# Performance work log

Measured on AMD Instinct MI355X. Metric: run time of the kernel, lower is better.

The kernel has to match this reference:

```python
import jax, jax.numpy as jnp
import numpy as np

N_HEADS = 16
NEG_INF = -1e30


def setup_inputs() -> dict:
    key = jax.random.key(0)
    ks = jax.random.split(key, 5)
    B, S, D = 2, 2048, 2048
    scale_w = 1.0 / np.sqrt(D)  # keep activations well-scaled
    return {
        "x": jax.random.normal(ks[0], (B, S, D), dtype=jnp.float32),
        "Wq": jax.random.normal(ks[1], (D, D), dtype=jnp.float32) * scale_w,
        "Wk": jax.random.normal(ks[2], (D, D), dtype=jnp.float32) * scale_w,
        "Wv": jax.random.normal(ks[3], (D, D), dtype=jnp.float32) * scale_w,
        "Wo": jax.random.normal(ks[4], (D, D), dtype=jnp.float32) * scale_w,
    }


def reference(x, Wq, Wk, Wv, Wo):
    # Blocked flash attention with online softmax is exactly causal softmax
    # attention; express it directly.
    B, S, D = x.shape
    H = N_HEADS
    dk = D // H
    scale = 1.0 / np.sqrt(dk)

    def heads(w):
        return (x @ w).reshape(B, S, H, dk)

    q = heads(Wq)  # [B,S,H,dk]
    k = heads(Wk)
    v = heads(Wv)

    scores = jnp.einsum("bqhd,bkhd->bhqk", q, k) * scale  # [B,H,S,S]
    causal = jnp.tril(jnp.ones((S, S), dtype=bool))
    scores = jnp.where(causal, scores, NEG_INF)
    p = jax.nn.softmax(scores, axis=-1)
    o = jnp.einsum("bhqk,bkhd->bqhd", p, v).reshape(B, S, D)
    return o @ Wo
```

## Files before the change

kernel.cpp:

```cpp
#include <hip/hip_runtime.h>
#include <hip/hip_bf16.h>

typedef short s16x8 __attribute__((ext_vector_type(8)));
typedef float f32x4 __attribute__((ext_vector_type(4)));
typedef unsigned short u16x4 __attribute__((ext_vector_type(4)));

#define MFMA16(a, b, c) __builtin_amdgcn_mfma_f32_16x16x32_bf16((a), (b), (c), 0, 0, 0)

__device__ __forceinline__ unsigned short f32_to_bf16(float f) {
  unsigned int u = __builtin_bit_cast(unsigned int, f);
  u += 0x7FFFu + ((u >> 16) & 1u);
  return (unsigned short)(u >> 16);
}

__device__ __forceinline__ void glds16(const unsigned short* g, unsigned short* l) {
  __builtin_amdgcn_global_load_lds(
      (const __attribute__((address_space(1))) void*)g,
      (__attribute__((address_space(3))) void*)l, 16, 0, 0);
}

__global__ void cvt_bf16_k(const float* __restrict__ in, unsigned short* __restrict__ out, int n4) {
  int i = blockIdx.x * 256 + threadIdx.x;
  if (i >= n4) return;
  float4 f = ((const float4*)in)[i];
  u16x4 o;
  o.x = f32_to_bf16(f.x); o.y = f32_to_bf16(f.y);
  o.z = f32_to_bf16(f.z); o.w = f32_to_bf16(f.w);
  ((u16x4*)out)[i] = o;
}

__global__ void cvt_t4_k(const float* __restrict__ Wq, const float* __restrict__ Wk,
                         const float* __restrict__ Wv, const float* __restrict__ Wo,
                         unsigned short* __restrict__ outQKV, unsigned short* __restrict__ outO,
                         int D) {
  int z = blockIdx.z;
  const float* in = (z == 0) ? Wq : (z == 1) ? Wk : (z == 2) ? Wv : Wo;
  unsigned short* out = (z < 3) ? (outQKV + (size_t)z * D * D) : outO;
  __shared__ float tile[32][33];
  int tx = threadIdx.x;
  int nt = D >> 5;
  int bx = blockIdx.x % nt;
  int by = blockIdx.x / nt;
  int r = tx >> 3, c4 = (tx & 7) * 4;
  int k0 = by * 32, n0 = bx * 32;
  float4 f = *(const float4*)(in + (size_t)(k0 + r) * D + n0 + c4);
  tile[r][c4 + 0] = f.x; tile[r][c4 + 1] = f.y;
  tile[r][c4 + 2] = f.z; tile[r][c4 + 3] = f.w;
  __syncthreads();
  u16x4 o;
  o.x = f32_to_bf16(tile[c4 + 0][r]);
  o.y = f32_to_bf16(tile[c4 + 1][r]);
  o.z = f32_to_bf16(tile[c4 + 2][r]);
  o.w = f32_to_bf16(tile[c4 + 3][r]);
  *(u16x4*)(out + (size_t)(n0 + r) * D + k0 + c4) = o;
}

template <int OUTF32>
__global__ __launch_bounds__(512, 4) void gemm3b(
    const unsigned short* __restrict__ A, const unsigned short* __restrict__ Bt,
    void* __restrict__ Cv, int M, int N, int K, int ldc) {
  __shared__ unsigned short As[3][256 * 32];
  __shared__ unsigned short Bs[3][128 * 32];
  int t = threadIdx.x, lane = t & 63, w = t >> 6;
  int r16 = lane & 15, kg = lane >> 4;
  int wm = w >> 1, wn = w & 1;
  int nbn = N >> 7;
  int bm = blockIdx.x / nbn, bn = blockIdx.x % nbn;
  const unsigned short* Ag = A + (size_t)bm * 256 * K;
  const unsigned short* Bg = Bt + (size_t)bn * 128 * K;

  const unsigned short* asrc[2];
  int aoff[2];
#pragma unroll
  for (int i = 0; i < 2; ++i) {
    int c = i * 512 + t;
    int row = c >> 2, sl = c & 3;
    asrc[i] = Ag + (size_t)row * K + ((sl ^ ((row >> 1) & 3)) * 8);
    aoff[i] = (i * 512 + (t & ~63)) * 8;
  }
  int brow = t >> 2;
  const unsigned short* bsrc = Bg + (size_t)brow * K + (((t & 3) ^ ((brow >> 1) & 3)) * 8);
  int boff = (t & ~63) * 8;

  auto STAGE = [&](int bi, int kt2) {
    int k0 = kt2 * 32;
    glds16(asrc[0] + k0, &As[bi][aoff[0]]);
    glds16(asrc[1] + k0, &As[bi][aoff[1]]);
    glds16(bsrc + k0, &Bs[bi][boff]);
  };

  f32x4 acc[4][4] = {};
  int nt = K >> 5;
  STAGE(0, 0);
  if (nt > 1) STAGE(1, 1);
  int cur = 0;
  for (int kt = 0; kt < nt; ++kt) {
    if (kt + 1 < nt) {
      asm volatile("s_waitcnt vmcnt(3)" ::: "memory");
    } else {
      asm volatile("s_waitcnt vmcnt(0)" ::: "memory");
    }
    __builtin_amdgcn_s_barrier();
    asm volatile("" ::: "memory");
    if (kt + 2 < nt) {
      int s2 = cur + 2; if (s2 >= 3) s2 -= 3;
      STAGE(s2, kt + 2);
    }
    const unsigned short* Al = As[cur];
    const unsigned short* Bl = Bs[cur];
    s16x8 af[4], bfr[4];
#pragma unroll
    for (int mf = 0; mf < 4; ++mf) {
      int row = wm * 64 + mf * 16 + r16;
      af[mf] = *(const s16x8*)&Al[row * 32 + ((kg ^ ((row >> 1) & 3)) * 8)];
    }
#pragma unroll
    for (int nf = 0; nf < 4; ++nf) {
      int row = wn * 64 + nf * 16 + r16;
      bfr[nf] = *(const s16x8*)&Bl[row * 32 + ((kg ^ ((row >> 1) & 3)) * 8)];
    }
    __builtin_amdgcn_s_setprio(1);
#pragma unroll
    for (int mf = 0; mf < 4; ++mf)
#pragma unroll
      for (int nf = 0; nf < 4; ++nf)
        acc[mf][nf] = MFMA16(af[mf], bfr[nf], acc[mf][nf]);
    __builtin_amdgcn_s_setprio(0);
    cur = (cur == 2) ? 0 : cur + 1;
  }
#pragma unroll
  for (int mf = 0; mf < 4; ++mf)
#pragma unroll
    for (int nf = 0; nf < 4; ++nf)
#pragma unroll
      for (int r = 0; r < 4; ++r) {
        int row = bm * 256 + wm * 64 + mf * 16 + kg * 4 + r;
        int col = bn * 128 + wn * 64 + nf * 16 + r16;
        if (OUTF32)
          ((float*)Cv)[(size_t)row * ldc + col] = acc[mf][nf][r];
        else
          ((unsigned short*)Cv)[(size_t)row * ldc + col] = f32_to_bf16(acc[mf][nf][r]);
      }
}

template <int OUTF32>
__global__ __launch_bounds__(512, 2) void gemm3(
    const unsigned short* __restrict__ A, const unsigned short* __restrict__ Bt,
    void* __restrict__ Cv, int M, int N, int K, int ldc) {
  __shared__ unsigned short As[3][256 * 64];
  __shared__ unsigned short Bs[3][128 * 64];
  int t = threadIdx.x, lane = t & 63, w = t >> 6;
  int r16 = lane & 15, kg = lane >> 4;
  int wm = w >> 1, wn = w & 1;
  int nbn = N >> 7;
  int bm = blockIdx.x / nbn, bn = blockIdx.x % nbn;
  const unsigned short* Ag = A + (size_t)bm * 256 * K;
  const unsigned short* Bg = Bt + (size_t)bn * 128 * K;

  const unsigned short* asrc[4];
  const unsigned short* bsrc[2];
  int aoff[4], boff[2];
#pragma unroll
  for (int i = 0; i < 4; ++i) {
    int c = i * 512 + t;
    int row = c >> 3, sl = c & 7;
    asrc[i] = Ag + (size_t)row * K + ((sl ^ (row & 7)) * 8);
    aoff[i] = (i * 512 + (t & ~63)) * 8;
  }
#pragma unroll
  for (int i = 0; i < 2; ++i) {
    int c = i * 512 + t;
    int row = c >> 3, sl = c & 7;
    bsrc[i] = Bg + (size_t)row * K + ((sl ^ (row & 7)) * 8);
    boff[i] = (i * 512 + (t & ~63)) * 8;
  }

  auto STAGE = [&](int bi, int kt2) {
    int k0 = kt2 * 64;
#pragma unroll
    for (int i = 0; i < 4; ++i) glds16(asrc[i] + k0, &As[bi][aoff[i]]);
#pragma unroll
    for (int i = 0; i < 2; ++i) glds16(bsrc[i] + k0, &Bs[bi][boff[i]]);
  };

  f32x4 acc[4][4] = {};
  int nt = K >> 6;
  STAGE(0, 0);
  if (nt > 1) STAGE(1, 1);
  int cur = 0;
  for (int kt = 0; kt < nt; ++kt) {
    if (kt + 1 < nt) {
      asm volatile("s_waitcnt vmcnt(6)" ::: "memory");
    } else {
      asm volatile("s_waitcnt vmcnt(0)" ::: "memory");
    }
    __builtin_amdgcn_s_barrier();
    asm volatile("" ::: "memory");
    if (kt + 2 < nt) {
      int s2 = cur + 2; if (s2 >= 3) s2 -= 3;
      STAGE(s2, kt + 2);
    }
    const unsigned short* Al = As[cur];
    s16x8 af[4][2], bfr[4][2];
#pragma unroll
    for (int mf = 0; mf < 4; ++mf) {
      int row = wm * 64 + mf * 16 + r16;
#pragma unroll
      for (int ks = 0; ks < 2; ++ks)
        af[mf][ks] = *(const s16x8*)&Al[row * 64 + (((ks * 4 + kg) ^ (row & 7)) * 8)];
    }
#pragma unroll
    for (int nf = 0; nf < 4; ++nf) {
      int row = wn * 64 + nf * 16 + r16;
#pragma unroll
      for (int ks = 0; ks < 2; ++ks)
        bfr[nf][ks] = *(const s16x8*)&Bs[cur][row * 64 + (((ks * 4 + kg) ^ (row & 7)) * 8)];
    }
    __builtin_amdgcn_s_setprio(1);
#pragma unroll
    for (int ks = 0; ks < 2; ++ks)
#pragma unroll
      for (int mf = 0; mf < 4; ++mf)
#pragma unroll
        for (int nf = 0; nf < 4; ++nf)
          acc[mf][nf] = MFMA16(af[mf][ks], bfr[nf][ks], acc[mf][nf]);
    __builtin_amdgcn_s_setprio(0);
    cur = (cur == 2) ? 0 : cur + 1;
  }
#pragma unroll
  for (int mf = 0; mf < 4; ++mf)
#pragma unroll
    for (int nf = 0; nf < 4; ++nf)
#pragma unroll
      for (int r = 0; r < 4; ++r) {
        int row = bm * 256 + wm * 64 + mf * 16 + kg * 4 + r;
        int col = bn * 128 + wn * 64 + nf * 16 + r16;
        if (OUTF32)
          ((float*)Cv)[(size_t)row * ldc + col] = acc[mf][nf][r];
        else
          ((unsigned short*)Cv)[(size_t)row * ldc + col] = f32_to_bf16(acc[mf][nf][r]);
      }
}

__global__ __launch_bounds__(256) void vtr_k(const unsigned short* __restrict__ V,
                                             unsigned short* __restrict__ Vt,
                                             int S, int ld) {
  __shared__ unsigned short T[32 * 128];
  int s0 = blockIdx.x * 32, h = blockIdx.y, b = blockIdx.z;
  int H = gridDim.y;
  int t = threadIdx.x;
  const unsigned short* src = V + (size_t)(b * S + s0) * ld + h * 128;
#pragma unroll
  for (int c = 0; c < 2; ++c) {
    int chunk = c * 256 + t;
    int row = chunk >> 4, slot = chunk & 15;
    glds16(src + (size_t)row * ld + slot * 8, &T[(c * 256 + (t & ~63)) * 8]);
  }
  __syncthreads();
  unsigned short* dst = Vt + ((size_t)(b * H + h) * (S >> 3) + (s0 >> 3)) * 1024;
#pragma unroll
  for (int c = 0; c < 2; ++c) {
    int oc = c * 256 + t;
    int sl = oc >> 7, d = oc & 127;
    s16x8 v;
#pragma unroll
    for (int j = 0; j < 8; ++j) v[j] = (short)T[(sl * 8 + j) * 128 + d];
    *(s16x8*)(dst + (size_t)oc * 8) = v;
  }
}

__global__ __launch_bounds__(512) void attn2_k(
    const unsigned short* __restrict__ Q, const unsigned short* __restrict__ Kx,
    const unsigned short* __restrict__ Vt, unsigned short* __restrict__ O,
    int S, int D, int Bn, int ld) {
  const float scale = 0.08838834764831843f;
  int hb = blockIdx.x;
  int h = hb / Bn, b = hb % Bn;
  int NQ = S >> 7;
  int qt = NQ - 1 - blockIdx.y;
  int H = D >> 7;
  int t = threadIdx.x, lane = t & 63, w = t >> 6;
  int r16 = lane & 15, kg = lane >> 4;
  const unsigned short* Qb  = Q + (size_t)b * S * ld + h * 128;
  const unsigned short* Kb  = Kx + (size_t)b * S * ld + h * 128;
  const unsigned short* Vtb = Vt + (size_t)(b * H + h) * (S >> 3) * 1024;

  __shared__ unsigned short Kbuf[2][64 * 128];
  __shared__ unsigned short Vbuf[2][64 * 128];
  __shared__ unsigned short Pl[8][16 * 64];

  auto STAGE = [&](int bufi, int kv0) {
    const unsigned short* Ksrc = Kb + (size_t)kv0 * ld;
#pragma unroll
    for (int c = 0; c < 2; ++c) {
      int chunk = c * 512 + t;
      int row = chunk >> 4, slot = chunk & 15;
      glds16(Ksrc + (size_t)row * ld + ((slot ^ (row & 7)) * 8),
             &Kbuf[bufi][(c * 512 + (t & ~63)) * 8]);
    }
    const unsigned short* Vsrc = Vtb + (size_t)(kv0 >> 3) * 1024;
#pragma unroll
    for (int c = 0; c < 2; ++c) {
      int chunk = c * 512 + t;
      glds16(Vsrc + (size_t)chunk * 8, &Vbuf[bufi][(c * 512 + (t & ~63)) * 8]);
    }
  };

  int W0 = qt * 128 + w * 16;
  int qg = W0 + r16;
  s16x8 qf[4];
#pragma unroll
  for (int ks = 0; ks < 4; ++ks)
    qf[ks] = *(const s16x8*)(Qb + (size_t)qg * ld + ks * 32 + kg * 8);
  f32x4 oacc[8] = {};
  float m_st = -1e30f, l_st = 0.f;
  int nt = (qt + 1) * 2;
  int cur = 0;
  STAGE(0, 0);
  __syncthreads();
  for (int it = 0; it < nt; ++it) {
    int kv0 = it * 64;
    if (it + 1 < nt) STAGE(cur ^ 1, (it + 1) * 64);
    const unsigned short* Kl = Kbuf[cur];
    const unsigned short* Vl = Vbuf[cur];
    if (kv0 <= W0 + 15) {
      f32x4 st4[4];
      __builtin_amdgcn_s_setprio(1);
#pragma unroll
      for (int kf = 0; kf < 4; ++kf) {
        f32x4 s = {};
#pragma unroll
        for (int ks = 0; ks < 4; ++ks) {
          int row = kf * 16 + r16;
          s16x8 kfr = *(const s16x8*)&Kl[row * 128 + (((ks * 4 + kg) ^ (row & 7)) * 8)];
          s = MFMA16(kfr, qf[ks], s);
        }
        st4[kf] = s;
      }
      __builtin_amdgcn_s_setprio(0);
      float p[4][4];
      float mx = -1e30f;
#pragma unroll
      for (int kf = 0; kf < 4; ++kf)
#pragma unroll
        for (int r = 0; r < 4; ++r) {
          int kvg = kv0 + kf * 16 + kg * 4 + r;
          float sv = st4[kf][r] * scale;
          sv = (kvg <= qg) ? sv : -1e30f;
          p[kf][r] = sv;
          mx = fmaxf(mx, sv);
        }
      mx = fmaxf(mx, __shfl_xor(mx, 16, 64));
      mx = fmaxf(mx, __shfl_xor(mx, 32, 64));
      bool skip = __all(mx <= m_st);
      float m_new = skip ? m_st : fmaxf(m_st, mx);
      float rs = 0.f;
#pragma unroll
      for (int kf = 0; kf < 4; ++kf)
#pragma unroll
        for (int r = 0; r < 4; ++r) {
          float e = __expf(p[kf][r] - m_new);
          p[kf][r] = e;
          rs += e;
        }
      rs += __shfl_xor(rs, 16, 64);
      rs += __shfl_xor(rs, 32, 64);
#pragma unroll
      for (int kf = 0; kf < 4; ++kf) {
        unsigned int lo = (unsigned int)f32_to_bf16(p[kf][0]) | ((unsigned int)f32_to_bf16(p[kf][1]) << 16);
        unsigned int hi = (unsigned int)f32_to_bf16(p[kf][2]) | ((unsigned int)f32_to_bf16(p[kf][3]) << 16);
        int sslot = 2 * kf + (kg >> 1);
        int base = r16 * 64 + ((sslot ^ (r16 & 7)) * 8) + (kg & 1) * 4;
        *(unsigned int*)&Pl[w][base]     = lo;
        *(unsigned int*)&Pl[w][base + 2] = hi;
      }
      asm volatile("s_waitcnt lgkmcnt(0)" ::: "memory");
      __builtin_amdgcn_sched_barrier(0);
      if (!skip) {
        float alpha = __expf(m_st - m_new);
        l_st = l_st * alpha + rs;
        m_st = m_new;
        float ar[4];
#pragma unroll
        for (int r = 0; r < 4; ++r) ar[r] = __shfl(alpha, kg * 4 + r, 64);
#pragma unroll
        for (int f = 0; f < 8; ++f)
#pragma unroll
          for (int r = 0; r < 4; ++r) oacc[f][r] *= ar[r];
      } else {
        l_st += rs;
      }
      __builtin_amdgcn_s_setprio(1);
#pragma unroll
      for (int tt = 0; tt < 2; ++tt) {
        s16x8 pf = *(const s16x8*)&Pl[w][r16 * 64 + (((4 * tt + kg) ^ (r16 & 7)) * 8)];
#pragma unroll
        for (int f = 0; f < 8; ++f) {
          s16x8 vf = *(const s16x8*)&Vl[((4 * tt + kg) * 128 + f * 16 + r16) * 8];
          oacc[f] = MFMA16(pf, vf, oacc[f]);
        }
      }
      __builtin_amdgcn_s_setprio(0);
    }
    __syncthreads();
    cur ^= 1;
  }
  float linv = 1.0f / l_st;
  float lr[4];
#pragma unroll
  for (int r = 0; r < 4; ++r) lr[r] = __shfl(linv, kg * 4 + r, 64);
#pragma unroll
  for (int f = 0; f < 8; ++f)
#pragma unroll
    for (int r = 0; r < 4; ++r) {
      size_t idx = ((size_t)b * S + W0 + kg * 4 + r) * D + h * 128 + f * 16 + r16;
      O[idx] = f32_to_bf16(oacc[f][r] * lr[r]);
    }
}

extern "C" void kernel_launch(void* const* d_in, const int* in_sizes, int n_in,
                              void* d_out, int out_size, void* d_ws, size_t ws_size,
                              hipStream_t stream) {
  const float* x  = (const float*)d_in[0];
  const float* Wq = (const float*)d_in[1];
  const float* Wk = (const float*)d_in[2];
  const float* Wv = (const float*)d_in[3];
  const float* Wo = (const float*)d_in[4];
  const int D = 2048, H = 16;
  const int M = in_sizes[0] / D;
  const int B = 2, S = M / B;
  const int LD = 3 * D;

  unsigned short* xb    = (unsigned short*)d_ws;
  unsigned short* Wqkvt = xb + (size_t)M * D;
  unsigned short* Wot   = Wqkvt + (size_t)3 * D * D;
  unsigned short* QKVb  = Wot + (size_t)D * D;
  unsigned short* Ob    = xb;
  unsigned short* VtA   = Wqkvt;

  int n4 = M * D / 4;
  cvt_bf16_k<<<(n4 + 255) / 256, 256, 0, stream>>>(x, xb, n4);
  int tgrid = (D / 32) * (D / 32);
  cvt_t4_k<<<dim3(tgrid, 1, 4), 256, 0, stream>>>(Wq, Wk, Wv, Wo, Wqkvt, Wot, D);

  gemm3b<0><<<(M / 256) * (LD / 128), 512, 0, stream>>>(xb, Wqkvt, QKVb, M, LD, D, LD);

  vtr_k<<<dim3(S / 32, H, B), 256, 0, stream>>>(QKVb + 2 * D, VtA, S, LD);

  attn2_k<<<dim3(H * B, S / 128), 512, 0, stream>>>(QKVb, QKVb + D, VtA, Ob, S, D, B, LD);

  gemm3<1><<<(M / 256) * (D / 128), 512, 0, stream>>>(Ob, Wot, d_out, M, D, D, D);
}
```

Baseline: 277.5 us.

## Retile output projection GEMM to 128x128 tiles with 256 threads and K=32 stages

Replaces the output-projection GEMM (256x128 tiles, 512 threads, K-step 64) with a 128x128 tile, 256-thread variant that stages 32-wide K slices in a triple buffer with a new XOR swizzle. For M=4096, N=2048 this doubles the block count from 128 to 256, which should fill more of the GPU's compute units, and the smaller LDS footprint allows three blocks per CU. The trade-off is less data reuse per tile, and twice as many barrier-synchronised K iterations with only one MFMA k-step each, which raises sync and load-issue overhead.

```diff
diff --git a/kernel.cpp b/kernel.cpp
--- a/kernel.cpp
+++ b/kernel.cpp
@@ -144,53 +144,48 @@
 }
 
 template <int OUTF32>
-__global__ __launch_bounds__(512, 2) void gemm3(
+__global__ __launch_bounds__(256, 3) void gemm3c(
     const unsigned short* __restrict__ A, const unsigned short* __restrict__ Bt,
     void* __restrict__ Cv, int M, int N, int K, int ldc) {
-  __shared__ unsigned short As[3][256 * 64];
-  __shared__ unsigned short Bs[3][128 * 64];
+  __shared__ unsigned short As[3][128 * 32];
+  __shared__ unsigned short Bs[3][128 * 32];
   int t = threadIdx.x, lane = t & 63, w = t >> 6;
   int r16 = lane & 15, kg = lane >> 4;
   int wm = w >> 1, wn = w & 1;
   int nbn = N >> 7;
   int bm = blockIdx.x / nbn, bn = blockIdx.x % nbn;
-  const unsigned short* Ag = A + (size_t)bm * 256 * K;
+  const unsigned short* Ag = A + (size_t)bm * 128 * K;
   const unsigned short* Bg = Bt + (size_t)bn * 128 * K;
 
-  const unsigned short* asrc[4];
+  const unsigned short* asrc[2];
   const unsigned short* bsrc[2];
-  int aoff[4], boff[2];
-#pragma unroll
-  for (int i = 0; i < 4; ++i) {
-    int c = i * 512 + t;
-    int row = c >> 3, sl = c & 7;
-    asrc[i] = Ag + (size_t)row * K + ((sl ^ (row & 7)) * 8);
-    aoff[i] = (i * 512 + (t & ~63)) * 8;
-  }
+  int doff[2];
 #pragma unroll
   for (int i = 0; i < 2; ++i) {
-    int c = i * 512 + t;
-    int row = c >> 3, sl = c & 7;
-    bsrc[i] = Bg + (size_t)row * K + ((sl ^ (row & 7)) * 8);
-    boff[i] = (i * 512 + (t & ~63)) * 8;
+    int c = i * 256 + t;
+    int row = c >> 2, sl = c & 3;
+    int col = (sl ^ ((row >> 1) & 3)) * 8;
+    asrc[i] = Ag + (size_t)row * K + col;
+    bsrc[i] = Bg + (size_t)row * K + col;
+    doff[i] = (i * 256 + (t & ~63)) * 8;
   }
 
   auto STAGE = [&](int bi, int kt2) {
-    int k0 = kt2 * 64;
-#pragma unroll
-    for (int i = 0; i < 4; ++i) glds16(asrc[i] + k0, &As[bi][aoff[i]]);
-#pragma unroll
-    for (int i = 0; i < 2; ++i) glds16(bsrc[i] + k0, &Bs[bi][boff[i]]);
+    int k0 = kt2 * 32;
+    glds16(asrc[0] + k0, &As[bi][doff[0]]);
+    glds16(asrc[1] + k0, &As[bi][doff[1]]);
+    glds16(bsrc[0] + k0, &Bs[bi][doff[0]]);
+    glds16(bsrc[1] + k0, &Bs[bi][doff[1]]);
   };
 
   f32x4 acc[4][4] = {};
-  int nt = K >> 6;
+  int nt = K >> 5;
   STAGE(0, 0);
   if (nt > 1) STAGE(1, 1);
   int cur = 0;
   for (int kt = 0; kt < nt; ++kt) {
     if (kt + 1 < nt) {
-      asm volatile("s_waitcnt vmcnt(6)" ::: "memory");
+      asm volatile("s_waitcnt vmcnt(4)" ::: "memory");
     } else {
       asm volatile("s_waitcnt vmcnt(0)" ::: "memory");
     }
@@ -201,29 +196,24 @@
       STAGE(s2, kt + 2);
     }
     const unsigned short* Al = As[cur];
-    s16x8 af[4][2], bfr[4][2];
+    const unsigned short* Bl = Bs[cur];
+    s16x8 af[4], bfr[4];
 #pragma unroll
     for (int mf = 0; mf < 4; ++mf) {
       int row = wm * 64 + mf * 16 + r16;
-#pragma unroll
-      for (int ks = 0; ks < 2; ++ks)
-        af[mf][ks] = *(const s16x8*)&Al[row * 64 + (((ks * 4 + kg) ^ (row & 7)) * 8)];
+      af[mf] = *(const s16x8*)&Al[row * 32 + ((kg ^ ((row >> 1) & 3)) * 8)];
     }
 #pragma unroll
     for (int nf = 0; nf < 4; ++nf) {
       int row = wn * 64 + nf * 16 + r16;
-#pragma unroll
-      for (int ks = 0; ks < 2; ++ks)
-        bfr[nf][ks] = *(const s16x8*)&Bs[cur][row * 64 + (((ks * 4 + kg) ^ (row & 7)) * 8)];
+      bfr[nf] = *(const s16x8*)&Bl[row * 32 + ((kg ^ ((row >> 1) & 3)) * 8)];
     }
     __builtin_amdgcn_s_setprio(1);
 #pragma unroll
-    for (int ks = 0; ks < 2; ++ks)
-#pragma unroll
-      for (int mf = 0; mf < 4; ++mf)
-#pragma unroll
-        for (int nf = 0; nf < 4; ++nf)
-          acc[mf][nf] = MFMA16(af[mf][ks], bfr[nf][ks], acc[mf][nf]);
+    for (int mf = 0; mf < 4; ++mf)
+#pragma unroll
+      for (int nf = 0; nf < 4; ++nf)
+        acc[mf][nf] = MFMA16(af[mf], bfr[nf], acc[mf][nf]);
     __builtin_amdgcn_s_setprio(0);
     cur = (cur == 2) ? 0 : cur + 1;
   }
@@ -233,7 +223,7 @@
     for (int nf = 0; nf < 4; ++nf)
 #pragma unroll
       for (int r = 0; r < 4; ++r) {
-        int row = bm * 256 + wm * 64 + mf * 16 + kg * 4 + r;
+        int row = bm * 128 + wm * 64 + mf * 16 + kg * 4 + r;
         int col = bn * 128 + wn * 64 + nf * 16 + r16;
         if (OUTF32)
           ((float*)Cv)[(size_t)row * ldc + col] = acc[mf][nf][r];
@@ -449,5 +439,5 @@
 
   attn2_k<<<dim3(H * B, S / 128), 512, 0, stream>>>(QKVb, QKVb + D, VtA, Ob, S, D, B, LD);
 
-  gemm3<1><<<(M / 256) * (D / 128), 512, 0, stream>>>(Ob, Wot, d_out, M, D, D, D);
-}
+  gemm3c<1><<<(M / 128) * (D / 128), 256, 0, stream>>>(Ob, Wot, d_out, M, D, D, D);
+}
```

Measured after the change: 281.1 us. No clear change (+1.3%).

## Give each attention wave two 16-row query tiles to reuse K/V fragments

Applied to the files above, without the earlier changes.

The attention kernel now runs 4 waves of 256 threads instead of 8 waves of 512. Each wave handles 32 query rows as two 16-row tiles, so every K and V fragment read from LDS feeds two MFMAs instead of one. This halves LDS fragment traffic per MFMA. In exchange it doubles per-wave accumulator registers, gives fewer waves to hide latency, and staging work per thread goes up.

```diff
diff --git a/kernel.cpp b/kernel.cpp
--- a/kernel.cpp
+++ b/kernel.cpp
@@ -269,7 +269,7 @@
   }
 }
 
-__global__ __launch_bounds__(512) void attn2_k(
+__global__ __launch_bounds__(256) void attn4_k(
     const unsigned short* __restrict__ Q, const unsigned short* __restrict__ Kx,
     const unsigned short* __restrict__ Vt, unsigned short* __restrict__ O,
     int S, int D, int Bn, int ld) {
@@ -287,33 +287,34 @@
 
   __shared__ unsigned short Kbuf[2][64 * 128];
   __shared__ unsigned short Vbuf[2][64 * 128];
-  __shared__ unsigned short Pl[8][16 * 64];
+  __shared__ unsigned short Pl[4][32 * 64];
 
   auto STAGE = [&](int bufi, int kv0) {
     const unsigned short* Ksrc = Kb + (size_t)kv0 * ld;
 #pragma unroll
-    for (int c = 0; c < 2; ++c) {
-      int chunk = c * 512 + t;
+    for (int c = 0; c < 4; ++c) {
+      int chunk = c * 256 + t;
       int row = chunk >> 4, slot = chunk & 15;
       glds16(Ksrc + (size_t)row * ld + ((slot ^ (row & 7)) * 8),
-             &Kbuf[bufi][(c * 512 + (t & ~63)) * 8]);
+             &Kbuf[bufi][(c * 256 + (t & ~63)) * 8]);
     }
     const unsigned short* Vsrc = Vtb + (size_t)(kv0 >> 3) * 1024;
 #pragma unroll
-    for (int c = 0; c < 2; ++c) {
-      int chunk = c * 512 + t;
-      glds16(Vsrc + (size_t)chunk * 8, &Vbuf[bufi][(c * 512 + (t & ~63)) * 8]);
+    for (int c = 0; c < 4; ++c) {
+      int chunk = c * 256 + t;
+      glds16(Vsrc + (size_t)chunk * 8, &Vbuf[bufi][(c * 256 + (t & ~63)) * 8]);
     }
   };
 
-  int W0 = qt * 128 + w * 16;
-  int qg = W0 + r16;
-  s16x8 qf[4];
-#pragma unroll
-  for (int ks = 0; ks < 4; ++ks)
-    qf[ks] = *(const s16x8*)(Qb + (size_t)qg * ld + ks * 32 + kg * 8);
-  f32x4 oacc[8] = {};
-  float m_st = -1e30f, l_st = 0.f;
+  int W0 = qt * 128 + w * 32;
+  s16x8 qf[2][4];
+#pragma unroll
+  for (int q2 = 0; q2 < 2; ++q2)
+#pragma unroll
+    for (int ks = 0; ks < 4; ++ks)
+      qf[q2][ks] = *(const s16x8*)(Qb + (size_t)(W0 + q2 * 16 + r16) * ld + ks * 32 + kg * 8);
+  f32x4 oacc[2][8] = {};
+  float m_st[2] = {-1e30f, -1e30f}, l_st[2] = {0.f, 0.f};
   int nt = (qt + 1) * 2;
   int cur = 0;
   STAGE(0, 0);
@@ -323,81 +324,92 @@
     if (it + 1 < nt) STAGE(cur ^ 1, (it + 1) * 64);
     const unsigned short* Kl = Kbuf[cur];
     const unsigned short* Vl = Vbuf[cur];
-    if (kv0 <= W0 + 15) {
-      f32x4 st4[4];
+    if (kv0 <= W0 + 31) {
+      f32x4 st[2][4];
+#pragma unroll
+      for (int q2 = 0; q2 < 2; ++q2)
+#pragma unroll
+        for (int kf = 0; kf < 4; ++kf) st[q2][kf] = f32x4{0.f, 0.f, 0.f, 0.f};
       __builtin_amdgcn_s_setprio(1);
 #pragma unroll
       for (int kf = 0; kf < 4; ++kf) {
-        f32x4 s = {};
+        int row = kf * 16 + r16;
 #pragma unroll
         for (int ks = 0; ks < 4; ++ks) {
-          int row = kf * 16 + r16;
           s16x8 kfr = *(const s16x8*)&Kl[row * 128 + (((ks * 4 + kg) ^ (row & 7)) * 8)];
-          s = MFMA16(kfr, qf[ks], s);
+          st[0][kf] = MFMA16(kfr, qf[0][ks], st[0][kf]);
+          st[1][kf] = MFMA16(kfr, qf[1][ks], st[1][kf]);
         }
-        st4[kf] = s;
       }
       __builtin_amdgcn_s_setprio(0);
-      float p[4][4];
-      float mx = -1e30f;
-#pragma unroll
-      for (int kf = 0; kf < 4; ++kf)
-#pragma unroll
-        for (int r = 0; r < 4; ++r) {
-          int kvg = kv0 + kf * 16 + kg * 4 + r;
-          float sv = st4[kf][r] * scale;
-          sv = (kvg <= qg) ? sv : -1e30f;
-          p[kf][r] = sv;
-          mx = fmaxf(mx, sv);
+      float p[2][4][4];
+#pragma unroll
+      for (int q2 = 0; q2 < 2; ++q2) {
+        int qg = W0 + q2 * 16 + r16;
+        float mx = -1e30f;
+#pragma unroll
+        for (int kf = 0; kf < 4; ++kf)
+#pragma unroll
+          for (int r = 0; r < 4; ++r) {
+            int kvg = kv0 + kf * 16 + kg * 4 + r;
+            float sv = st[q2][kf][r] * scale;
+            sv = (kvg <= qg) ? sv : -1e30f;
+            p[q2][kf][r] = sv;
+            mx = fmaxf(mx, sv);
+          }
+        mx = fmaxf(mx, __shfl_xor(mx, 16, 64));
+        mx = fmaxf(mx, __shfl_xor(mx, 32, 64));
+        bool skip = __all(mx <= m_st[q2]);
+        float m_new = skip ? m_st[q2] : fmaxf(m_st[q2], mx);
+        float rs = 0.f;
+#pragma unroll
+        for (int kf = 0; kf < 4; ++kf)
+#pragma unroll
+          for (int r = 0; r < 4; ++r) {
+            float e = __expf(p[q2][kf][r] - m_new);
+            p[q2][kf][r] = e;
+            rs += e;
+          }
+        rs += __shfl_xor(rs, 16, 64);
+        rs += __shfl_xor(rs, 32, 64);
+        if (!skip) {
+          float alpha = __expf(m_st[q2] - m_new);
+          l_st[q2] = l_st[q2] * alpha + rs;
+          m_st[q2] = m_new;
+          float ar[4];
+#pragma unroll
+          for (int r = 0; r < 4; ++r) ar[r] = __shfl(alpha, kg * 4 + r, 64);
+#pragma unroll
+          for (int f = 0; f < 8; ++f)
+#pragma unroll
+            for (int r = 0; r < 4; ++r) oacc[q2][f][r] *= ar[r];
+        } else {
+          l_st[q2] += rs;
         }
-      mx = fmaxf(mx, __shfl_xor(mx, 16, 64));
-      mx = fmaxf(mx, __shfl_xor(mx, 32, 64));
-      bool skip = __all(mx <= m_st);
-      float m_new = skip ? m_st : fmaxf(m_st, mx);
-      float rs = 0.f;
-#pragma unroll
-      for (int kf = 0; kf < 4; ++kf)
-#pragma unroll
-        for (int r = 0; r < 4; ++r) {
-          float e = __expf(p[kf][r] - m_new);
-          p[kf][r] = e;
-          rs += e;
+        int prow = q2 * 16 + r16;
+#pragma unroll
+        for (int kf = 0; kf < 4; ++kf) {
+          unsigned int lo = (unsigned int)f32_to_bf16(p[q2][kf][0]) | ((unsigned int)f32_to_bf16(p[q2][kf][1]) << 16);
+          unsigned int hi = (unsigned int)f32_to_bf16(p[q2][kf][2]) | ((unsigned int)f32_to_bf16(p[q2][kf][3]) << 16);
+          int sslot = 2 * kf + (kg >> 1);
+          int base = prow * 64 + ((sslot ^ (prow & 7)) * 8) + (kg & 1) * 4;
+          *(unsigned int*)&Pl[w][base]     = lo;
+          *(unsigned int*)&Pl[w][base + 2] = hi;
         }
-      rs += __shfl_xor(rs, 16, 64);
-      rs += __shfl_xor(rs, 32, 64);
-#pragma unroll
-      for (int kf = 0; kf < 4; ++kf) {
-        unsigned int lo = (unsigned int)f32_to_bf16(p[kf][0]) | ((unsigned int)f32_to_bf16(p[kf][1]) << 16);
-        unsigned int hi = (unsigned int)f32_to_bf16(p[kf][2]) | ((unsigned int)f32_to_bf16(p[kf][3]) << 16);
-        int sslot = 2 * kf + (kg >> 1);
-        int base = r16 * 64 + ((sslot ^ (r16 & 7)) * 8) + (kg & 1) * 4;
-        *(unsigned int*)&Pl[w][base]     = lo;
-        *(unsigned int*)&Pl[w][base + 2] = hi;
       }
       asm volatile("s_waitcnt lgkmcnt(0)" ::: "memory");
       __builtin_amdgcn_sched_barrier(0);
-      if (!skip) {
-        float alpha = __expf(m_st - m_new);
-        l_st = l_st * alpha + rs;
-        m_st = m_new;
-        float ar[4];
-#pragma unroll
-        for (int r = 0; r < 4; ++r) ar[r] = __shfl(alpha, kg * 4 + r, 64);
-#pragma unroll
-        for (int f = 0; f < 8; ++f)
-#pragma unroll
-          for (int r = 0; r < 4; ++r) oacc[f][r] *= ar[r];
-      } else {
-        l_st += rs;
-      }
       __builtin_amdgcn_s_setprio(1);
 #pragma unroll
       for (int tt = 0; tt < 2; ++tt) {
-        s16x8 pf = *(const s16x8*)&Pl[w][r16 * 64 + (((4 * tt + kg) ^ (r16 & 7)) * 8)];
+        int soff = (((4 * tt + kg) ^ (r16 & 7)) * 8);
+        s16x8 pf0 = *(const s16x8*)&Pl[w][r16 * 64 + soff];
+        s16x8 pf1 = *(const s16x8*)&Pl[w][(16 + r16) * 64 + soff];
 #pragma unroll
         for (int f = 0; f < 8; ++f) {
           s16x8 vf = *(const s16x8*)&Vl[((4 * tt + kg) * 128 + f * 16 + r16) * 8];
-          oacc[f] = MFMA16(pf, vf, oacc[f]);
+          oacc[0][f] = MFMA16(pf0, vf, oacc[0][f]);
+          oacc[1][f] = MFMA16(pf1, vf, oacc[1][f]);
         }
       }
       __builtin_amdgcn_s_setprio(0);
@@ -405,17 +417,20 @@
     __syncthreads();
     cur ^= 1;
   }
-  float linv = 1.0f / l_st;
-  float lr[4];
-#pragma unroll
-  for (int r = 0; r < 4; ++r) lr[r] = __shfl(linv, kg * 4 + r, 64);
-#pragma unroll
-  for (int f = 0; f < 8; ++f)
-#pragma unroll
-    for (int r = 0; r < 4; ++r) {
-      size_t idx = ((size_t)b * S + W0 + kg * 4 + r) * D + h * 128 + f * 16 + r16;
-      O[idx] = f32_to_bf16(oacc[f][r] * lr[r]);
-    }
+#pragma unroll
+  for (int q2 = 0; q2 < 2; ++q2) {
+    float linv = 1.0f / l_st[q2];
+    float lr[4];
+#pragma unroll
+    for (int r = 0; r < 4; ++r) lr[r] = __shfl(linv, kg * 4 + r, 64);
+#pragma unroll
+    for (int f = 0; f < 8; ++f)
+#pragma unroll
+      for (int r = 0; r < 4; ++r) {
+        size_t idx = ((size_t)b * S + W0 + q2 * 16 + kg * 4 + r) * D + h * 128 + f * 16 + r16;
+        O[idx] = f32_to_bf16(oacc[q2][f][r] * lr[r]);
+      }
+  }
 }
 
 extern "C" void kernel_launch(void* const* d_in, const int* in_sizes, int n_in,
@@ -447,7 +462,7 @@
 
   vtr_k<<<dim3(S / 32, H, B), 256, 0, stream>>>(QKVb + 2 * D, VtA, S, LD);
 
-  attn2_k<<<dim3(H * B, S / 128), 512, 0, stream>>>(QKVb, QKVb + D, VtA, Ob, S, D, B, LD);
+  attn4_k<<<dim3(H * B, S / 128), 256, 0, stream>>>(QKVb, QKVb + D, VtA, Ob, S, D, B, LD);
 
   gemm3<1><<<(M / 256) * (D / 128), 512, 0, stream>>>(Ob, Wot, d_out, M, D, D, D);
 }
```

After: 304.4 us. 9.7% more time.
